# Optimization experiments

Hardware: AMD Instinct MI355X
Metric: run time of the kernel (lower is better)

The kernel has to match this reference:

```python
import jax, jax.numpy as jnp
import numpy as np

N_NODES = 50000
N_EDGES = 800000
IN_CH = 128
OUT_CH = 64
BN_EPS = 1e-5


def setup_inputs() -> dict:
    key = jax.random.key(0)
    k1, k2, k3 = jax.random.split(key, 3)
    x = jax.random.normal(k1, (N_NODES, IN_CH), dtype=jnp.float32)
    edge_index = jax.random.randint(k2, (2, N_EDGES), 0, N_NODES, dtype=jnp.int64)
    W = jax.random.normal(k3, (IN_CH, OUT_CH), dtype=jnp.float32) / np.sqrt(IN_CH)
    bias = jnp.zeros((OUT_CH,), dtype=jnp.float32)
    gamma = jnp.ones((OUT_CH,), dtype=jnp.float32)
    beta = jnp.zeros((OUT_CH,), dtype=jnp.float32)
    return {"x": x, "edge_index": edge_index, "W": W, "bias": bias,
            "gamma": gamma, "beta": beta}


def reference(x, edge_index, W, bias, gamma, beta):
    N = x.shape[0]
    # Linear transform first (GCNConv order): [N, out]
    h = x @ W
    # Add self-loops
    loops = jnp.arange(N, dtype=edge_index.dtype)
    src = jnp.concatenate([edge_index[0], loops])  # [E+N]
    dst = jnp.concatenate([edge_index[1], loops])
    # Symmetric GCN normalization: deg^{-1/2}[src] * deg^{-1/2}[dst]
    ones = jnp.ones(dst.shape[0], dtype=h.dtype)
    deg = jax.ops.segment_sum(ones, dst, num_segments=N)
    dinv = jnp.where(deg > 0, jax.lax.rsqrt(deg), 0.0)
    norm = dinv[src] * dinv[dst]  # [E+N]
    # Gather, scale, scatter-add
    msgs = h[src] * norm[:, None]  # [E+N, out]
    agg = jax.ops.segment_sum(msgs, dst, num_segments=N) + bias  # [N, out]
    # tanh activation
    a = jnp.tanh(agg)
    # BatchNorm over node dim (training mode, biased var)
    mean = jnp.mean(a, axis=0)
    var = jnp.mean(jnp.square(a - mean), axis=0)
    return gamma * (a - mean) * jax.lax.rsqrt(var + BN_EPS) + beta
```

## Files before the change

kernel.cpp:

```cpp
#include <hip/hip_runtime.h>
#include <hip/hip_bf16.h>
#include <math.h>

#define N_NODES 50000
#define N_EDGES 800000
#define IN_CH 128
#define OUT_CH 64
#define BN_EPS 1e-5f
#define CAP 64

typedef __attribute__((ext_vector_type(8))) short short8;
typedef __attribute__((ext_vector_type(4))) float f32x4;

__device__ __forceinline__ float bf16u_to_f32(uint u) { return __uint_as_float(u << 16); }

__device__ __forceinline__ ushort f32_to_bf16(float f) {
    uint u = __float_as_uint(f);
    uint r = (u + 0x7fff + ((u >> 16) & 1)) >> 16;
    return (ushort)r;
}

__global__ void fill_slots_kernel(const int4* __restrict__ esrc4, const int4* __restrict__ edst4,
                                  int* __restrict__ cnt, ushort* __restrict__ slot, int E4) {
    int i = blockIdx.x * blockDim.x + threadIdx.x;
    if (i < E4) {
        int4 s = esrc4[i];
        int4 d = edst4[i];
        int p;
        p = atomicAdd(&cnt[d.x], 1); if (p < CAP) slot[d.x * CAP + p] = (ushort)s.x;
        p = atomicAdd(&cnt[d.y], 1); if (p < CAP) slot[d.y * CAP + p] = (ushort)s.y;
        p = atomicAdd(&cnt[d.z], 1); if (p < CAP) slot[d.z * CAP + p] = (ushort)s.z;
        p = atomicAdd(&cnt[d.w], 1); if (p < CAP) slot[d.w * CAP + p] = (ushort)s.w;
    }
}

__global__ void prep_kernel(const int* __restrict__ cnt, float* __restrict__ dinv,
                            float* __restrict__ sums, int N) {
    int i = blockIdx.x * blockDim.x + threadIdx.x;
    if (i < N) dinv[i] = rsqrtf((float)(cnt[i] + 1));
    if (i < 128) sums[i] = 0.0f;
}

#define XPAD 136
__global__ __launch_bounds__(256) void gemm_mfma_kernel(const float* __restrict__ x,
                                                        const float* __restrict__ W,
                                                        ushort* __restrict__ hb, int N) {
    __shared__ ushort xs[64 * XPAD];
    __shared__ ushort wt[64 * XPAD];
    int t = threadIdx.x;
    int lane = t & 63;
    int w = t >> 6;
    int nn = lane & 15;
    int quad = lane >> 4;
    int row0 = blockIdx.x * 64;

#pragma unroll
    for (int i = 0; i < 32; ++i) {
        int wlin = t + 256 * i;
        int k = wlin >> 6, n = wlin & 63;
        wt[n * XPAD + k] = f32_to_bf16(W[wlin]);
    }
#pragma unroll
    for (int i = 0; i < 8; ++i) {
        int linear4 = t + 256 * i;
        int r = linear4 >> 5;
        int c4 = linear4 & 31;
        int gr = row0 + r; if (gr >= N) gr = N - 1;
        float4 v = *(const float4*)(x + (size_t)gr * IN_CH + c4 * 4);
        ushort u0 = f32_to_bf16(v.x), u1 = f32_to_bf16(v.y);
        ushort u2 = f32_to_bf16(v.z), u3 = f32_to_bf16(v.w);
        uint2 packed = make_uint2((uint)u0 | ((uint)u1 << 16), (uint)u2 | ((uint)u3 << 16));
        *(uint2*)&xs[r * XPAD + c4 * 4] = packed;
    }
    __syncthreads();

    short8 bfrag[4][4];
#pragma unroll
    for (int t2 = 0; t2 < 4; ++t2)
#pragma unroll
        for (int c = 0; c < 4; ++c)
            bfrag[t2][c] = *(const short8*)&wt[(16 * t2 + nn) * XPAD + 32 * c + quad * 8];

    f32x4 acc[4] = {{0.f, 0.f, 0.f, 0.f}, {0.f, 0.f, 0.f, 0.f},
                    {0.f, 0.f, 0.f, 0.f}, {0.f, 0.f, 0.f, 0.f}};
#pragma unroll
    for (int c = 0; c < 4; ++c) {
        short8 afrag = *(const short8*)&xs[(16 * w + nn) * XPAD + 32 * c + quad * 8];
#pragma unroll
        for (int t2 = 0; t2 < 4; ++t2)
            acc[t2] = __builtin_amdgcn_mfma_f32_16x16x32_bf16(afrag, bfrag[t2][c], acc[t2], 0, 0, 0);
    }

#pragma unroll
    for (int t2 = 0; t2 < 4; ++t2) {
#pragma unroll
        for (int r = 0; r < 4; ++r) {
            int row = row0 + 16 * w + quad * 4 + r;
            if (row < N) hb[(size_t)row * OUT_CH + 16 * t2 + nn] = f32_to_bf16(acc[t2][r]);
        }
    }
}

__global__ __launch_bounds__(256) void gather_fused_kernel(const int* __restrict__ cnt,
                                                           const ushort* __restrict__ slot,
                                                           const float* __restrict__ dinv,
                                                           const ushort* __restrict__ hb,
                                                           const float* __restrict__ bias,
                                                           float* __restrict__ out,
                                                           float* __restrict__ sums, int N) {
    int t = threadIdx.x;
    int lane = t & 63;
    int wid = (blockIdx.x * blockDim.x + t) >> 6;
    int nw = (gridDim.x * blockDim.x) >> 6;
    float bias_c = bias[lane];
    float ssum = 0.f, ssq = 0.f;

    for (int d = wid; d < N; d += nw) {
        float dd = dinv[d];
        float acc = bf16u_to_f32(hb[(size_t)d * OUT_CH + lane]) * dd * dd;
        int m = cnt[d]; if (m > CAP) m = CAP;
        int sv = __builtin_nontemporal_load(&slot[(size_t)d * CAP + lane]);
        if (lane >= m) sv = 0;
        float dv = dinv[sv];
        int j = 0;
        for (; j + 3 < m; j += 4) {
            int s0 = __shfl(sv, j + 0); float w0 = __shfl(dv, j + 0);
            int s1 = __shfl(sv, j + 1); float w1 = __shfl(dv, j + 1);
            int s2 = __shfl(sv, j + 2); float w2 = __shfl(dv, j + 2);
            int s3 = __shfl(sv, j + 3); float w3 = __shfl(dv, j + 3);
            uint h0 = hb[(size_t)s0 * OUT_CH + lane];
            uint h1 = hb[(size_t)s1 * OUT_CH + lane];
            uint h2 = hb[(size_t)s2 * OUT_CH + lane];
            uint h3 = hb[(size_t)s3 * OUT_CH + lane];
            acc += bf16u_to_f32(h0) * (w0 * dd);
            acc += bf16u_to_f32(h1) * (w1 * dd);
            acc += bf16u_to_f32(h2) * (w2 * dd);
            acc += bf16u_to_f32(h3) * (w3 * dd);
        }
        for (; j < m; ++j) {
            int s = __shfl(sv, j);
            float ww = __shfl(dv, j) * dd;
            acc += bf16u_to_f32(hb[(size_t)s * OUT_CH + lane]) * ww;
        }
        float v = tanhf(acc + bias_c);
        out[(size_t)d * OUT_CH + lane] = v;
        ssum += v;
        ssq += v * v;
    }

    __shared__ float ls[256];
    __shared__ float ls2[256];
    ls[t] = ssum; ls2[t] = ssq;
    __syncthreads();
    if (t < 128) { ls[t] += ls[t + 128]; ls2[t] += ls2[t + 128]; }
    __syncthreads();
    if (t < 64) {
        atomicAdd(&sums[t], ls[t] + ls[t + 64]);
        atomicAdd(&sums[64 + t], ls2[t] + ls2[t + 64]);
    }
}

__global__ __launch_bounds__(256) void bn_apply_kernel(float4* __restrict__ a,
                                                       const float* __restrict__ sums,
                                                       const float* __restrict__ gamma,
                                                       const float* __restrict__ beta, int total4) {
    int c0 = (threadIdx.x * 4) & 63;
    const float invN = 1.0f / (float)N_NODES;
    float4 scale, shift;
    {
        float m0 = sums[c0 + 0] * invN, m1 = sums[c0 + 1] * invN;
        float m2 = sums[c0 + 2] * invN, m3 = sums[c0 + 3] * invN;
        float v0 = sums[64 + c0 + 0] * invN - m0 * m0;
        float v1 = sums[64 + c0 + 1] * invN - m1 * m1;
        float v2 = sums[64 + c0 + 2] * invN - m2 * m2;
        float v3 = sums[64 + c0 + 3] * invN - m3 * m3;
        scale.x = gamma[c0 + 0] * rsqrtf(v0 + BN_EPS);
        scale.y = gamma[c0 + 1] * rsqrtf(v1 + BN_EPS);
        scale.z = gamma[c0 + 2] * rsqrtf(v2 + BN_EPS);
        scale.w = gamma[c0 + 3] * rsqrtf(v3 + BN_EPS);
        shift.x = beta[c0 + 0] - m0 * scale.x;
        shift.y = beta[c0 + 1] - m1 * scale.y;
        shift.z = beta[c0 + 2] - m2 * scale.z;
        shift.w = beta[c0 + 3] - m3 * scale.w;
    }
    int stride = gridDim.x * blockDim.x;
    for (int idx = blockIdx.x * blockDim.x + threadIdx.x; idx < total4; idx += stride) {
        float4 v = a[idx];
        v.x = v.x * scale.x + shift.x;
        v.y = v.y * scale.y + shift.y;
        v.z = v.z * scale.z + shift.z;
        v.w = v.w * scale.w + shift.w;
        a[idx] = v;
    }
}

extern "C" void kernel_launch(void* const* d_in, const int* in_sizes, int n_in,
                              void* d_out, int out_size, void* d_ws, size_t ws_size,
                              hipStream_t stream) {
    const float* x     = (const float*)d_in[0];
    const int*   eidx  = (const int*)d_in[1];
    const float* W     = (const float*)d_in[2];
    const float* bias  = (const float*)d_in[3];
    const float* gamma = (const float*)d_in[4];
    const float* beta  = (const float*)d_in[5];
    float* out = (float*)d_out;

    const int4* esrc4 = (const int4*)eidx;
    const int4* edst4 = (const int4*)(eidx + N_EDGES);

    ushort* hb   = (ushort*)d_ws;
    int*   cnt   = (int*)(hb + (size_t)N_NODES * OUT_CH);
    float* sums  = (float*)(cnt + N_NODES);
    float* dinv  = sums + 128;
    ushort* slot = (ushort*)(dinv + N_NODES);

    hipMemsetAsync(cnt, 0, (size_t)N_NODES * 4, stream);
    fill_slots_kernel<<<(N_EDGES / 4 + 255) / 256, 256, 0, stream>>>(esrc4, edst4, cnt, slot, N_EDGES / 4);
    prep_kernel<<<(N_NODES + 255) / 256, 256, 0, stream>>>(cnt, dinv, sums, N_NODES);
    gemm_mfma_kernel<<<(N_NODES + 63) / 64, 256, 0, stream>>>(x, W, hb, N_NODES);
    gather_fused_kernel<<<2048, 256, 0, stream>>>(cnt, slot, dinv, hb, bias, out, sums, N_NODES);
    bn_apply_kernel<<<512, 256, 0, stream>>>((float4*)out, sums, gamma, beta, N_NODES * OUT_CH / 4);
}
```

Baseline: 237.2 us.

## Prescale h by dinv in GEMM, vectorize gather with 16B loads and prefetch

The GEMM epilogue multiplies each row of h by dinv, so the gather no longer needs per-edge source weights. The gather is restructured so each lane loads a 16-byte chunk covering eight bf16 channels from 8 edges at a time. Partial sums are combined with a butterfly of xor-shuffles, and the next node's metadata is software-prefetched. A zero padding row lets out-of-range edges be read without branches. The change also adds a fast exp/rcp tanh, nontemporal stores for slot writes and a launch bounds occupancy hint, at the cost of extra shuffle work and slightly lower tanh accuracy.

```diff
diff --git a/kernel.cpp b/kernel.cpp
--- a/kernel.cpp
+++ b/kernel.cpp
@@ -18,6 +18,15 @@
     uint u = __float_as_uint(f);
     uint r = (u + 0x7fff + ((u >> 16) & 1)) >> 16;
     return (ushort)r;
+}
+
+__device__ __forceinline__ float fast_tanh(float x) {
+    float xa = fminf(x, 30.0f);
+    float e;
+    asm("v_exp_f32 %0, %1" : "=v"(e) : "v"(xa * 2.8853900817779268f));
+    float inv;
+    asm("v_rcp_f32 %0, %1" : "=v"(inv) : "v"(e + 1.0f));
+    return (e - 1.0f) * inv;
 }
 
 __global__ void fill_slots_kernel(const int4* __restrict__ esrc4, const int4* __restrict__ edst4,
@@ -27,23 +36,25 @@
         int4 s = esrc4[i];
         int4 d = edst4[i];
         int p;
-        p = atomicAdd(&cnt[d.x], 1); if (p < CAP) slot[d.x * CAP + p] = (ushort)s.x;
-        p = atomicAdd(&cnt[d.y], 1); if (p < CAP) slot[d.y * CAP + p] = (ushort)s.y;
-        p = atomicAdd(&cnt[d.z], 1); if (p < CAP) slot[d.z * CAP + p] = (ushort)s.z;
-        p = atomicAdd(&cnt[d.w], 1); if (p < CAP) slot[d.w * CAP + p] = (ushort)s.w;
+        p = atomicAdd(&cnt[d.x], 1); if (p < CAP) __builtin_nontemporal_store((ushort)s.x, &slot[d.x * CAP + p]);
+        p = atomicAdd(&cnt[d.y], 1); if (p < CAP) __builtin_nontemporal_store((ushort)s.y, &slot[d.y * CAP + p]);
+        p = atomicAdd(&cnt[d.z], 1); if (p < CAP) __builtin_nontemporal_store((ushort)s.z, &slot[d.z * CAP + p]);
+        p = atomicAdd(&cnt[d.w], 1); if (p < CAP) __builtin_nontemporal_store((ushort)s.w, &slot[d.w * CAP + p]);
     }
 }
 
 __global__ void prep_kernel(const int* __restrict__ cnt, float* __restrict__ dinv,
-                            float* __restrict__ sums, int N) {
+                            float* __restrict__ sums, ushort* __restrict__ hb, int N) {
     int i = blockIdx.x * blockDim.x + threadIdx.x;
     if (i < N) dinv[i] = rsqrtf((float)(cnt[i] + 1));
     if (i < 128) sums[i] = 0.0f;
+    if (i < OUT_CH) hb[(size_t)N * OUT_CH + i] = 0;
 }
 
 #define XPAD 136
 __global__ __launch_bounds__(256) void gemm_mfma_kernel(const float* __restrict__ x,
                                                         const float* __restrict__ W,
+                                                        const float* __restrict__ dinv,
                                                         ushort* __restrict__ hb, int N) {
     __shared__ ushort xs[64 * XPAD];
     __shared__ ushort wt[64 * XPAD];
@@ -91,62 +102,128 @@
             acc[t2] = __builtin_amdgcn_mfma_f32_16x16x32_bf16(afrag, bfrag[t2][c], acc[t2], 0, 0, 0);
     }
 
+    int rbase = row0 + 16 * w + quad * 4;
+    float dv[4];
+#pragma unroll
+    for (int r = 0; r < 4; ++r) dv[r] = (rbase + r < N) ? dinv[rbase + r] : 0.f;
 #pragma unroll
     for (int t2 = 0; t2 < 4; ++t2) {
 #pragma unroll
         for (int r = 0; r < 4; ++r) {
-            int row = row0 + 16 * w + quad * 4 + r;
-            if (row < N) hb[(size_t)row * OUT_CH + 16 * t2 + nn] = f32_to_bf16(acc[t2][r]);
-        }
-    }
-}
-
-__global__ __launch_bounds__(256) void gather_fused_kernel(const int* __restrict__ cnt,
-                                                           const ushort* __restrict__ slot,
-                                                           const float* __restrict__ dinv,
-                                                           const ushort* __restrict__ hb,
-                                                           const float* __restrict__ bias,
-                                                           float* __restrict__ out,
-                                                           float* __restrict__ sums, int N) {
+            int row = rbase + r;
+            if (row < N) hb[(size_t)row * OUT_CH + 16 * t2 + nn] = f32_to_bf16(acc[t2][r] * dv[r]);
+        }
+    }
+}
+
+__global__ __launch_bounds__(256, 8) void gather_fused_kernel(const int* __restrict__ cnt,
+                                                              const ushort* __restrict__ slot,
+                                                              const float* __restrict__ dinv,
+                                                              const ushort* __restrict__ hb,
+                                                              const float* __restrict__ bias,
+                                                              float* __restrict__ out,
+                                                              float* __restrict__ sums, int N) {
     int t = threadIdx.x;
     int lane = t & 63;
+    int g = lane >> 3;
+    int sub = lane & 7;
+    int cidx = 8 * sub + (((g & 1) << 2) | (g & 2) | ((g >> 2) & 1));
     int wid = (blockIdx.x * blockDim.x + t) >> 6;
     int nw = (gridDim.x * blockDim.x) >> 6;
-    float bias_c = bias[lane];
+    float bias_c = bias[cidx];
     float ssum = 0.f, ssq = 0.f;
 
-    for (int d = wid; d < N; d += nw) {
-        float dd = dinv[d];
-        float acc = bf16u_to_f32(hb[(size_t)d * OUT_CH + lane]) * dd * dd;
-        int m = cnt[d]; if (m > CAP) m = CAP;
-        int sv = __builtin_nontemporal_load(&slot[(size_t)d * CAP + lane]);
-        if (lane >= m) sv = 0;
-        float dv = dinv[sv];
-        int j = 0;
-        for (; j + 3 < m; j += 4) {
-            int s0 = __shfl(sv, j + 0); float w0 = __shfl(dv, j + 0);
-            int s1 = __shfl(sv, j + 1); float w1 = __shfl(dv, j + 1);
-            int s2 = __shfl(sv, j + 2); float w2 = __shfl(dv, j + 2);
-            int s3 = __shfl(sv, j + 3); float w3 = __shfl(dv, j + 3);
-            uint h0 = hb[(size_t)s0 * OUT_CH + lane];
-            uint h1 = hb[(size_t)s1 * OUT_CH + lane];
-            uint h2 = hb[(size_t)s2 * OUT_CH + lane];
-            uint h3 = hb[(size_t)s3 * OUT_CH + lane];
-            acc += bf16u_to_f32(h0) * (w0 * dd);
-            acc += bf16u_to_f32(h1) * (w1 * dd);
-            acc += bf16u_to_f32(h2) * (w2 * dd);
-            acc += bf16u_to_f32(h3) * (w3 * dd);
-        }
-        for (; j < m; ++j) {
-            int s = __shfl(sv, j);
-            float ww = __shfl(dv, j) * dd;
-            acc += bf16u_to_f32(hb[(size_t)s * OUT_CH + lane]) * ww;
-        }
-        float v = tanhf(acc + bias_c);
-        out[(size_t)d * OUT_CH + lane] = v;
+#define ISSUE(J, H0, H1) do {                                              \
+        int e0 = (J) + g, e1 = e0 + 8;                                     \
+        int i0 = e0 - 1; i0 = (i0 < 0) ? 0 : i0;                           \
+        int s0 = __shfl(sv, i0);                                           \
+        int s1 = __shfl(sv, e1 - 1);                                       \
+        s0 = (e0 == 0) ? d : s0;                                           \
+        s0 = (e0 < M) ? s0 : N_NODES;                                      \
+        s1 = (e1 < M) ? s1 : N_NODES;                                      \
+        H0 = *(const uint4*)(hb + ((size_t)s0 << 6) + (sub << 3));         \
+        H1 = *(const uint4*)(hb + ((size_t)s1 << 6) + (sub << 3));         \
+    } while (0)
+
+#define CONSUME(H)                                                          \
+        a0 += __uint_as_float((H).x << 16); a1 += __uint_as_float((H).x & 0xffff0000u); \
+        a2 += __uint_as_float((H).y << 16); a3 += __uint_as_float((H).y & 0xffff0000u); \
+        a4 += __uint_as_float((H).z << 16); a5 += __uint_as_float((H).z & 0xffff0000u); \
+        a6 += __uint_as_float((H).w << 16); a7 += __uint_as_float((H).w & 0xffff0000u);
+
+    int d = wid;
+    float dd_n = 0.f;
+    int m_n = 0, sv_n = 0;
+    if (d < N) {
+        dd_n = dinv[d];
+        m_n = cnt[d];
+        sv_n = __builtin_nontemporal_load(&slot[(size_t)d * CAP + lane]);
+    }
+
+    while (d < N) {
+        float dd = dd_n;
+        int m = m_n; if (m > CAP) m = CAP;
+        int sv = sv_n;
+        int M = m + 1;
+
+        int dn = d + nw;
+        if (dn < N) {
+            dd_n = dinv[dn];
+            m_n = cnt[dn];
+            sv_n = __builtin_nontemporal_load(&slot[(size_t)dn * CAP + lane]);
+        }
+
+        float a0 = 0.f, a1 = 0.f, a2 = 0.f, a3 = 0.f;
+        float a4 = 0.f, a5 = 0.f, a6 = 0.f, a7 = 0.f;
+
+        uint4 h0, h1;
+        ISSUE(0, h0, h1);
+        for (int j = 16; j < M; j += 16) {
+            uint4 n0, n1;
+            ISSUE(j, n0, n1);
+            CONSUME(h0); CONSUME(h1);
+            h0 = n0; h1 = n1;
+        }
+        CONSUME(h0); CONSUME(h1);
+
+        float b0, b1, b2, b3;
+        {
+            float s0 = a0 + __shfl_xor(a0, 8);
+            float s1 = a1 + __shfl_xor(a1, 8);
+            float s2 = a2 + __shfl_xor(a2, 8);
+            float s3 = a3 + __shfl_xor(a3, 8);
+            float s4 = a4 + __shfl_xor(a4, 8);
+            float s5 = a5 + __shfl_xor(a5, 8);
+            float s6 = a6 + __shfl_xor(a6, 8);
+            float s7 = a7 + __shfl_xor(a7, 8);
+            bool hi = (g & 1);
+            b0 = hi ? s4 : s0; b1 = hi ? s5 : s1; b2 = hi ? s6 : s2; b3 = hi ? s7 : s3;
+        }
+        float c0, c1;
+        {
+            float s0 = b0 + __shfl_xor(b0, 16);
+            float s1 = b1 + __shfl_xor(b1, 16);
+            float s2 = b2 + __shfl_xor(b2, 16);
+            float s3 = b3 + __shfl_xor(b3, 16);
+            bool hi = (g & 2);
+            c0 = hi ? s2 : s0; c1 = hi ? s3 : s1;
+        }
+        float total;
+        {
+            float s0 = c0 + __shfl_xor(c0, 32);
+            float s1 = c1 + __shfl_xor(c1, 32);
+            total = (g & 4) ? s1 : s0;
+        }
+
+        float v = fast_tanh(fmaf(dd, total, bias_c));
+        out[(size_t)d * OUT_CH + cidx] = v;
         ssum += v;
         ssq += v * v;
-    }
+
+        d = dn;
+    }
+#undef ISSUE
+#undef CONSUME
 
     __shared__ float ls[256];
     __shared__ float ls2[256];
@@ -155,8 +232,8 @@
     if (t < 128) { ls[t] += ls[t + 128]; ls2[t] += ls2[t + 128]; }
     __syncthreads();
     if (t < 64) {
-        atomicAdd(&sums[t], ls[t] + ls[t + 64]);
-        atomicAdd(&sums[64 + t], ls2[t] + ls2[t + 64]);
+        atomicAdd(&sums[cidx], ls[t] + ls[t + 64]);
+        atomicAdd(&sums[64 + cidx], ls2[t] + ls2[t + 64]);
     }
 }
 
@@ -209,15 +286,15 @@
     const int4* edst4 = (const int4*)(eidx + N_EDGES);
 
     ushort* hb   = (ushort*)d_ws;
-    int*   cnt   = (int*)(hb + (size_t)N_NODES * OUT_CH);
+    int*   cnt   = (int*)(hb + (size_t)(N_NODES + 1) * OUT_CH);
     float* sums  = (float*)(cnt + N_NODES);
     float* dinv  = sums + 128;
     ushort* slot = (ushort*)(dinv + N_NODES);
 
     hipMemsetAsync(cnt, 0, (size_t)N_NODES * 4, stream);
     fill_slots_kernel<<<(N_EDGES / 4 + 255) / 256, 256, 0, stream>>>(esrc4, edst4, cnt, slot, N_EDGES / 4);
-    prep_kernel<<<(N_NODES + 255) / 256, 256, 0, stream>>>(cnt, dinv, sums, N_NODES);
-    gemm_mfma_kernel<<<(N_NODES + 63) / 64, 256, 0, stream>>>(x, W, hb, N_NODES);
+    prep_kernel<<<(N_NODES + 255) / 256, 256, 0, stream>>>(cnt, dinv, sums, hb, N_NODES);
+    gemm_mfma_kernel<<<(N_NODES + 63) / 64, 256, 0, stream>>>(x, W, dinv, hb, N_NODES);
     gather_fused_kernel<<<2048, 256, 0, stream>>>(cnt, slot, dinv, hb, bias, out, sums, N_NODES);
     bn_apply_kernel<<<512, 256, 0, stream>>>((float4*)out, sums, gamma, beta, N_NODES * OUT_CH / 4);
 }
```

After: 204.3 us. 1.16x faster.
